# Optimization experiments

Measured on AMD Instinct MI355X. Metric: run time of the kernel, lower is better.

## Reference

```python
import jax, jax.numpy as jnp
import numpy as np

N = 100000          # nodes
E = 3200000         # edges (avg degree 32)
C = 64              # classes
NUM_CORR = 10
ALPHA_CORR = 0.979
NUM_SMOOTH = 10
ALPHA_SMOOTH = 0.756


def setup_inputs() -> dict:
    key = jax.random.key(0)
    k1, k2, k3, k4, k5 = jax.random.split(key, 5)
    # soft predictions: rows sum to 1 (asserted in the torch code)
    y_soft = jax.nn.softmax(jax.random.normal(k1, (N, C), dtype=jnp.float32), axis=-1)
    labels = jax.random.randint(k2, (N,), 0, C)
    y_true = jax.nn.one_hot(labels, C, dtype=jnp.float32)
    src = jax.random.randint(k3, (E,), 0, N)
    dst = jax.random.randint(k4, (E,), 0, N)
    mask = jax.random.uniform(k5, (N,)) < 0.5
    return {"y_soft": y_soft, "y_true": y_true, "src": src, "dst": dst, "mask": mask}


def _propagate(y, src, dst, norm, num_layers, alpha, lo, hi):
    # DAD: y <- clip(last + alpha * D^-1/2 A D^-1/2 y, lo, hi) repeated
    last = (1.0 - alpha) * y
    for _ in range(num_layers):
        y = norm * y                                            # D^-1/2 y
        h = jax.ops.segment_sum(y[src], dst, num_segments=N)    # A (SpMM via copy_u/sum)
        y = alpha * h * norm                                    # alpha D^-1/2 (.)
        y = jnp.clip(last + y, lo, hi)                          # post_step clamp
    return y


def reference(y_soft, y_true, src, dst, mask):
    dt = y_soft.dtype
    degs = jnp.clip(jax.ops.segment_sum(jnp.ones((E,), dt), dst, num_segments=N), 1.0, None)
    norm = (degs ** -0.5)[:, None]                              # [N,1]
    m = mask[:, None]

    # ---- correct (autoscale=True) ----
    error = jnp.where(m, y_true - y_soft, jnp.zeros((), dt))    # zero off-mask
    smoothed_error = _propagate(error, src, dst, norm, NUM_CORR, ALPHA_CORR, -1.0, 1.0)
    numel = jnp.sum(mask).astype(dt)
    sigma = jnp.sum(jnp.abs(error)) / numel                     # error is 0 off-mask
    scale = sigma / jnp.sum(jnp.abs(smoothed_error), axis=1, keepdims=True)
    scale = jnp.where(jnp.isinf(scale) | (scale > 1000.0), jnp.ones((), dt), scale)
    result = y_soft + scale * smoothed_error
    result = jnp.where(jnp.isnan(result), y_soft, result)

    # ---- smooth ----
    y = jnp.where(m, y_true, result)                            # y_soft[mask] = y_true
    out = _propagate(y, src, dst, norm, NUM_SMOOTH, ALPHA_SMOOTH, 0.0, 1.0)
    return out
```

## Files before the change

### kernel.cpp

```cpp
#include <hip/hip_runtime.h>
#include <hip/hip_bf16.h>

#define NN 100000
#define EE 3200000
#define CC 64
#define NC (NN*CC)
#define ERR_BLOCKS 6250
#define NB 391
#define TILE 8192
#define NTILE 391

__device__ __forceinline__ float ldf(const void* p, long i, int isbf) {
    if (isbf) {
        unsigned int u = ((const unsigned short*)p)[i];
        return __uint_as_float(u << 16);
    }
    return ((const float*)p)[i];
}

__device__ __forceinline__ float wave_sum(float a) {
    for (int m = 1; m < 64; m <<= 1) a += __shfl_xor(a, m, 64);
    return a;
}

__device__ __forceinline__ unsigned pack_bf16(float a, float b) {
    unsigned ua = __float_as_uint(a); ua = (ua + 0x7FFFu + ((ua >> 16) & 1u)) >> 16;
    unsigned ub = __float_as_uint(b); ub = (ub + 0x7FFFu + ((ub >> 16) & 1u)) >> 16;
    return ua | (ub << 16);
}

__global__ void detect_kernel(const void* ytrue, const void* mask, int* flags) {
    int t = threadIdx.x;
    const unsigned int* w = (const unsigned int*)ytrue;
    int nb = 0, nm = 0;
    for (int i = t; i < 16384; i += 256)
        if ((w[i] & 0xFFFFu) == 0x3F80u) nb = 1;
    const unsigned char* mb = (const unsigned char*)mask;
    for (int i = t; i < 4096; i += 256)
        if ((i & 3) != 0 && mb[i] != 0) nm = 1;
    if (nb) atomicOr(&flags[0], 1);
    if (nm) atomicOr(&flags[1], 1);
}

__global__ void prep_kernel(const void* ytrue, const void* mask, const int* flags,
                            int* __restrict__ label, float* __restrict__ mask01) {
    int gt = blockIdx.x * blockDim.x + threadIdx.x;
    int node = gt >> 6, lane = gt & 63;
    if (node >= NN) return;
    int isbf = flags[0];
    float tv = ldf(ytrue, (long)node * CC + lane, isbf);
    unsigned long long b = __ballot(tv > 0.5f);
    if (lane == 0) {
        label[node] = (b == 0ull) ? 0 : (__ffsll((long long)b) - 1);
        int mv = flags[1] ? (int)((const unsigned char*)mask)[node] : ((const int*)mask)[node];
        mask01[node] = mv ? 1.f : 0.f;
    }
}

__global__ void histA_kernel(const int* __restrict__ dst, int* __restrict__ bucket_tot) {
    __shared__ int hist[NB];
    int t = threadIdx.x;
    for (int b = t; b < NB; b += 256) hist[b] = 0;
    __syncthreads();
    int e0 = blockIdx.x * TILE;
    int n = EE - e0; if (n > TILE) n = TILE;
    for (int k = t; k < n; k += 256)
        atomicAdd(&hist[dst[e0 + k] >> 8], 1);
    __syncthreads();
    for (int b = t; b < NB; b += 256)
        if (hist[b]) atomicAdd(&bucket_tot[b], hist[b]);
}

__global__ void bscan_kernel(const int* __restrict__ bucket_tot,
                             int* __restrict__ bucket_base, int* __restrict__ bucket_fill) {
    int t = threadIdx.x;
    __shared__ int sm[512];
    int v = (t < NB) ? bucket_tot[t] : 0;
    sm[t] = v; __syncthreads();
    for (int off = 1; off < 512; off <<= 1) {
        int x = (t >= off) ? sm[t - off] : 0;
        __syncthreads();
        sm[t] += x;
        __syncthreads();
    }
    int ex = sm[t] - v;
    if (t <= NB) { bucket_base[t] = ex; bucket_fill[t] = ex; }
}

__global__ void __launch_bounds__(512)
binA_kernel(const int* __restrict__ src, const int* __restrict__ dst,
            int* __restrict__ bucket_fill, uint2* __restrict__ tmp) {
    __shared__ uint2 stage[TILE];
    __shared__ int hist[512], hofs[512], curL[512], gbase[512];
    __shared__ int sm[512];
    int t = threadIdx.x;
    int e0 = blockIdx.x * TILE;
    int n = EE - e0; if (n > TILE) n = TILE;

    hist[t] = 0;
    __syncthreads();
    for (int k = t; k < n; k += 512)
        atomicAdd(&hist[dst[e0 + k] >> 8], 1);
    __syncthreads();
    int v = hist[t];
    sm[t] = v; __syncthreads();
    for (int off = 1; off < 512; off <<= 1) {
        int x = (t >= off) ? sm[t - off] : 0;
        __syncthreads();
        sm[t] += x;
        __syncthreads();
    }
    hofs[t] = sm[t] - v;
    curL[t] = sm[t] - v;
    __syncthreads();
    for (int k = t; k < n; k += 512) {
        int s = src[e0 + k], d = dst[e0 + k];
        int b = d >> 8;
        int p = atomicAdd(&curL[b], 1);
        stage[p] = make_uint2((unsigned)s, (unsigned)d);
    }
    if (t < NB) {
        int c = hist[t];
        gbase[t] = c ? atomicAdd(&bucket_fill[t], c) : 0;
    }
    __syncthreads();
    for (int k = t; k < n; k += 512) {
        uint2 pr = stage[k];
        int b = (int)(pr.y >> 8);
        tmp[gbase[b] + (k - hofs[b])] = pr;
    }
}

__global__ void __launch_bounds__(256)
csrB_kernel(const uint2* __restrict__ tmp, const int* __restrict__ bucket_base,
            int* __restrict__ row_ptr, float* __restrict__ norm, int* __restrict__ csr_src) {
    __shared__ int deg[256], cur[256], sm[256];
    int t = threadIdx.x, b = blockIdx.x;
    int ebeg = bucket_base[b], eend = bucket_base[b + 1];
    deg[t] = 0;
    __syncthreads();
    for (int i = ebeg + t; i < eend; i += 256)
        atomicAdd(&deg[tmp[i].y & 255u], 1);
    __syncthreads();
    int v = deg[t];
    sm[t] = v; __syncthreads();
    for (int off = 1; off < 256; off <<= 1) {
        int x = (t >= off) ? sm[t - off] : 0;
        __syncthreads();
        sm[t] += x;
        __syncthreads();
    }
    int lofs = sm[t] - v;
    int node = b * 256 + t;
    if (node < NN) {
        row_ptr[node] = ebeg + lofs;
        int d = v; if (d < 1) d = 1;
        norm[node] = rsqrtf((float)d);
    }
    if (b == NB - 1 && t == 0) row_ptr[NN] = EE;
    cur[t] = lofs;
    __syncthreads();
    for (int i = ebeg + t; i < eend; i += 256) {
        uint2 pr = tmp[i];
        int p = atomicAdd(&cur[pr.y & 255u], 1);
        csr_src[ebeg + p] = (int)pr.x;
    }
}

__global__ void err_kernel(const void* ysoft, const int* flags, const int* __restrict__ label,
                           const float* __restrict__ mask01, const float* __restrict__ norm,
                           float* __restrict__ base, unsigned* __restrict__ curn,
                           float* __restrict__ err_part) {
    int i4 = blockIdx.x * 256 + threadIdx.x;
    int node = i4 >> 4;
    int isbf = flags[0];
    float m = mask01[node];
    int lab = label[node];
    float nrm = norm[node];
    int c0 = (i4 & 15) * 4;
    float4 e;
    if (isbf) {
        ushort4 u = ((const ushort4*)ysoft)[i4];
        e.x = __uint_as_float((unsigned)u.x << 16);
        e.y = __uint_as_float((unsigned)u.y << 16);
        e.z = __uint_as_float((unsigned)u.z << 16);
        e.w = __uint_as_float((unsigned)u.w << 16);
    } else {
        e = ((const float4*)ysoft)[i4];
    }
    e.x = (m != 0.f) ? ((c0 + 0 == lab) ? 1.f : 0.f) - e.x : 0.f;
    e.y = (m != 0.f) ? ((c0 + 1 == lab) ? 1.f : 0.f) - e.y : 0.f;
    e.z = (m != 0.f) ? ((c0 + 2 == lab) ? 1.f : 0.f) - e.z : 0.f;
    e.w = (m != 0.f) ? ((c0 + 3 == lab) ? 1.f : 0.f) - e.w : 0.f;
    ((float4*)base)[i4] = e;
    ((uint2*)curn)[i4] = make_uint2(pack_bf16(e.x * nrm, e.y * nrm),
                                    pack_bf16(e.z * nrm, e.w * nrm));
    float a = fabsf(e.x) + fabsf(e.y) + fabsf(e.z) + fabsf(e.w);
    a = wave_sum(a);
    __shared__ float sm[4];
    if ((threadIdx.x & 63) == 0) sm[threadIdx.x >> 6] = a;
    __syncthreads();
    if (threadIdx.x == 0) err_part[blockIdx.x] = sm[0] + sm[1] + sm[2] + sm[3];
}

__global__ void reduce_kernel(const float* __restrict__ mask01,
                              const float* __restrict__ err_part, float* __restrict__ scal) {
    int t = threadIdx.x;
    float s0 = 0.f, s1 = 0.f;
    for (int i = t; i < NN; i += 1024) s0 += mask01[i];
    for (int i = t; i < ERR_BLOCKS; i += 1024) s1 += err_part[i];
    __shared__ float a0[1024], a1[1024];
    a0[t] = s0; a1[t] = s1; __syncthreads();
    for (int s = 512; s > 0; s >>= 1) {
        if (t < s) { a0[t] += a0[t + s]; a1[t] += a1[t + s]; }
        __syncthreads();
    }
    if (t == 0) { scal[0] = a0[0]; scal[1] = a1[0]; }
}

__global__ void gather_kernel(const int* __restrict__ row_ptr, const int* __restrict__ csr_src,
                              const unsigned* __restrict__ curn, const float* __restrict__ base,
                              const float* __restrict__ norm, void* __restrict__ out,
                              float* __restrict__ rowsum, const int* flags,
                              float alpha, float lo, float hi, int mode) {
    int gt = blockIdx.x * blockDim.x + threadIdx.x;
    int node = gt >> 6, lane = gt & 63;
    if (node >= NN) return;
    int hl = lane & 31;
    int half = lane >> 5;
    int beg = row_ptr[node], end = row_ptr[node + 1];

    float nrm = norm[node];
    long i2 = (long)node * 32 + hl;
    float2 b2;
    {
        const float* bp = base + i2 * 2;
        b2.x = __builtin_nontemporal_load(bp);
        b2.y = __builtin_nontemporal_load(bp + 1);
    }

    float acc0 = 0.f, acc1 = 0.f, acc2 = 0.f, acc3 = 0.f;
    for (int eb = beg; eb < end; eb += 64) {
        int ne = end - eb; if (ne > 64) ne = 64;
        int sv = (eb + lane < end) ? __builtin_nontemporal_load(csr_src + eb + lane) : 0;
        int j = 0;
        for (; j + 15 < ne; j += 16) {
            int s0 = __shfl(sv, j + 0  + half, 64);
            int s1 = __shfl(sv, j + 2  + half, 64);
            int s2 = __shfl(sv, j + 4  + half, 64);
            int s3 = __shfl(sv, j + 6  + half, 64);
            int s4 = __shfl(sv, j + 8  + half, 64);
            int s5 = __shfl(sv, j + 10 + half, 64);
            int s6 = __shfl(sv, j + 12 + half, 64);
            int s7 = __shfl(sv, j + 14 + half, 64);
            unsigned w0 = curn[(long)s0 * 32 + hl];
            unsigned w1 = curn[(long)s1 * 32 + hl];
            unsigned w2 = curn[(long)s2 * 32 + hl];
            unsigned w3 = curn[(long)s3 * 32 + hl];
            unsigned w4 = curn[(long)s4 * 32 + hl];
            unsigned w5 = curn[(long)s5 * 32 + hl];
            unsigned w6 = curn[(long)s6 * 32 + hl];
            unsigned w7 = curn[(long)s7 * 32 + hl];
            acc0 += __uint_as_float(w0 << 16) + __uint_as_float(w2 << 16)
                  + __uint_as_float(w4 << 16) + __uint_as_float(w6 << 16);
            acc1 += __uint_as_float(w0 & 0xFFFF0000u) + __uint_as_float(w2 & 0xFFFF0000u)
                  + __uint_as_float(w4 & 0xFFFF0000u) + __uint_as_float(w6 & 0xFFFF0000u);
            acc2 += __uint_as_float(w1 << 16) + __uint_as_float(w3 << 16)
                  + __uint_as_float(w5 << 16) + __uint_as_float(w7 << 16);
            acc3 += __uint_as_float(w1 & 0xFFFF0000u) + __uint_as_float(w3 & 0xFFFF0000u)
                  + __uint_as_float(w5 & 0xFFFF0000u) + __uint_as_float(w7 & 0xFFFF0000u);
        }
        for (; j + 7 < ne; j += 8) {
            int s0 = __shfl(sv, j + 0 + half, 64);
            int s1 = __shfl(sv, j + 2 + half, 64);
            int s2 = __shfl(sv, j + 4 + half, 64);
            int s3 = __shfl(sv, j + 6 + half, 64);
            unsigned w0 = curn[(long)s0 * 32 + hl];
            unsigned w1 = curn[(long)s1 * 32 + hl];
            unsigned w2 = curn[(long)s2 * 32 + hl];
            unsigned w3 = curn[(long)s3 * 32 + hl];
            acc0 += __uint_as_float(w0 << 16) + __uint_as_float(w2 << 16);
            acc1 += __uint_as_float(w0 & 0xFFFF0000u) + __uint_as_float(w2 & 0xFFFF0000u);
            acc2 += __uint_as_float(w1 << 16) + __uint_as_float(w3 << 16);
            acc3 += __uint_as_float(w1 & 0xFFFF0000u) + __uint_as_float(w3 & 0xFFFF0000u);
        }
        for (; j < ne; j += 2) {
            int jj = j + half;
            float wt = (jj < ne) ? 1.f : 0.f;
            int s = __shfl(sv, (jj < ne) ? jj : j, 64);
            unsigned w = curn[(long)s * 32 + hl];
            acc0 += wt * __uint_as_float(w << 16);
            acc1 += wt * __uint_as_float(w & 0xFFFF0000u);
        }
    }
    acc0 += acc2; acc1 += acc3;
    acc0 += __shfl_xor(acc0, 32, 64);
    acc1 += __shfl_xor(acc1, 32, 64);

    float v0 = (1.f - alpha) * b2.x + alpha * nrm * acc0;
    float v1 = (1.f - alpha) * b2.y + alpha * nrm * acc1;
    v0 = v0 < lo ? lo : (v0 > hi ? hi : v0);
    v1 = v1 < lo ? lo : (v1 > hi ? hi : v1);

    if (mode == 1) {
        float contrib = (lane < 32) ? (fabsf(v0) + fabsf(v1)) : 0.f;
        float rs = wave_sum(contrib);
        if (lane == 0) rowsum[node] = rs;
        if (lane < 32) {
            float* op = (float*)out + i2 * 2;
            __builtin_nontemporal_store(v0, op);
            __builtin_nontemporal_store(v1, op + 1);
        }
    } else if (mode == 0) {
        if (lane < 32)
            __builtin_nontemporal_store(pack_bf16(v0 * nrm, v1 * nrm), (unsigned*)out + i2);
    } else {
        if (lane < 32) {
            if (flags[0]) __builtin_nontemporal_store(pack_bf16(v0, v1), (unsigned*)out + i2);
            else {
                float* op = (float*)out + i2 * 2;
                __builtin_nontemporal_store(v0, op);
                __builtin_nontemporal_store(v1, op + 1);
            }
        }
    }
}

__global__ void y0_kernel(const void* ysoft, const int* flags, const int* __restrict__ label,
                          const float* __restrict__ mask01, const float* __restrict__ rowsum,
                          const float* __restrict__ scal,
                          const float* __restrict__ norm, const float* __restrict__ smoothed,
                          float* __restrict__ base, unsigned* __restrict__ curn) {
    int i4 = blockIdx.x * 256 + threadIdx.x;
    int node = i4 >> 4;
    int isbf = flags[0];
    float m = mask01[node];
    int lab = label[node];
    float nrm = norm[node];
    float sigma = scal[1] / scal[0];
    float sc = sigma / rowsum[node];
    if (isinf(sc) || sc > 1000.f) sc = 1.f;
    int c0 = (i4 & 15) * 4;
    float4 ys;
    if (isbf) {
        ushort4 u = ((const ushort4*)ysoft)[i4];
        ys.x = __uint_as_float((unsigned)u.x << 16);
        ys.y = __uint_as_float((unsigned)u.y << 16);
        ys.z = __uint_as_float((unsigned)u.z << 16);
        ys.w = __uint_as_float((unsigned)u.w << 16);
    } else {
        ys = ((const float4*)ysoft)[i4];
    }
    float4 sm = ((const float4*)smoothed)[i4];
    float rx = ys.x + sc * sm.x; if (isnan(rx)) rx = ys.x;
    float ry = ys.y + sc * sm.y; if (isnan(ry)) ry = ys.y;
    float rz = ys.z + sc * sm.z; if (isnan(rz)) rz = ys.z;
    float rw = ys.w + sc * sm.w; if (isnan(rw)) rw = ys.w;
    float4 y;
    y.x = (m != 0.f) ? ((c0 + 0 == lab) ? 1.f : 0.f) : rx;
    y.y = (m != 0.f) ? ((c0 + 1 == lab) ? 1.f : 0.f) : ry;
    y.z = (m != 0.f) ? ((c0 + 2 == lab) ? 1.f : 0.f) : rz;
    y.w = (m != 0.f) ? ((c0 + 3 == lab) ? 1.f : 0.f) : rw;
    ((float4*)base)[i4] = y;
    ((uint2*)curn)[i4] = make_uint2(pack_bf16(y.x * nrm, y.y * nrm),
                                    pack_bf16(y.z * nrm, y.w * nrm));
}

extern "C" void kernel_launch(void* const* d_in, const int* in_sizes, int n_in,
                              void* d_out, int out_size, void* d_ws, size_t ws_size,
                              hipStream_t stream) {
    const void* ysoft = d_in[0];
    const void* ytrue = d_in[1];
    const int* src = (const int*)d_in[2];
    const int* dst = (const int*)d_in[3];
    const void* mask = d_in[4];

    char* ws = (char*)d_ws;
    int*   flags       = (int*)ws;
    float* scal        = (float*)(ws + 64);
    int*   bucket_tot  = (int*)(ws + 4096);
    size_t ZERO_BYTES  = 16384;
    int*   bucket_base = (int*)(ws + 16384);
    int*   bucket_fill = (int*)(ws + 20480);
    float* err_part    = (float*)(ws + 24576);

    size_t off = 24576 + (size_t)ERR_BLOCKS * 4;
    off = (off + 255) & ~(size_t)255;
    int*   label   = (int*)(ws + off);   off += (size_t)NN * 4;
    float* mask01  = (float*)(ws + off); off += (size_t)NN * 4;
    float* norm    = (float*)(ws + off); off += (size_t)NN * 4;
    float* rowsum  = (float*)(ws + off); off += (size_t)NN * 4;
    int*   row_ptr = (int*)(ws + off);   off += (size_t)(NN + 1) * 4;
    off = (off + 255) & ~(size_t)255;
    int*   csr_src = (int*)(ws + off);   off += (size_t)EE * 4;
    off = (off + 255) & ~(size_t)255;
    float*    base     = (float*)(ws + off);    off += (size_t)NC * 4;
    float*    smoothed = (float*)(ws + off);    off += (size_t)NC * 4;
    unsigned* bufA     = (unsigned*)(ws + off); off += (size_t)NC * 2;
    unsigned* bufB     = (unsigned*)(ws + off); off += (size_t)NC * 2;
    uint2* tmp = (uint2*)base;

    hipMemsetAsync(ws, 0, ZERO_BYTES, stream);

    detect_kernel<<<1, 256, 0, stream>>>(ytrue, mask, flags);
    prep_kernel<<<(NN * 64 + 255) / 256, 256, 0, stream>>>(ytrue, mask, flags, label, mask01);
    histA_kernel<<<NTILE, 256, 0, stream>>>(dst, bucket_tot);
    bscan_kernel<<<1, 512, 0, stream>>>(bucket_tot, bucket_base, bucket_fill);
    binA_kernel<<<NTILE, 512, 0, stream>>>(src, dst, bucket_fill, tmp);
    csrB_kernel<<<NB, 256, 0, stream>>>(tmp, bucket_base, row_ptr, norm, csr_src);
    err_kernel<<<ERR_BLOCKS, 256, 0, stream>>>(ysoft, flags, label, mask01, norm, base, bufA, err_part);
    reduce_kernel<<<1, 1024, 0, stream>>>(mask01, err_part, scal);

    const int gather_blocks = (NN * 64 + 255) / 256;

    unsigned* cur = bufA; unsigned* nxt = bufB;
    for (int l = 0; l < 10; l++) {
        int mode = (l < 9) ? 0 : 1;
        void* o = (l < 9) ? (void*)nxt : (void*)smoothed;
        gather_kernel<<<gather_blocks, 256, 0, stream>>>(row_ptr, csr_src, cur, base, norm, o,
                                                         rowsum, flags, 0.979f, -1.f, 1.f, mode);
        unsigned* t = cur; cur = nxt; nxt = t;
    }

    y0_kernel<<<ERR_BLOCKS, 256, 0, stream>>>(ysoft, flags, label, mask01, rowsum, scal, norm,
                                              smoothed, base, bufA);

    cur = bufA; nxt = bufB;
    for (int l = 0; l < 10; l++) {
        int mode = (l < 9) ? 0 : 3;
        void* o = (l < 9) ? (void*)nxt : (void*)d_out;
        gather_kernel<<<gather_blocks, 256, 0, stream>>>(row_ptr, csr_src, cur, base, norm, o,
                                                         rowsum, flags, 0.756f, 0.f, 1.f, mode);
        unsigned* t = cur; cur = nxt; nxt = t;
    }
}
```

Before: 1.453 ms.

## Sort edges by source then destination and store base term in bf16

The CSR build becomes a two-pass bucket sort: edges are first binned by source, then re-binned by destination using per-tile offsets. Chunked loops with barriers make the ordering close to stable, so each row's neighbour list ends up roughly sorted by source. That sorting aims to improve cache locality of the gather's feature reads. Separately, the (1-alpha)*base term is now stored as bf16 instead of fp32, halving that read in every gather iteration. The cost is extra preprocessing kernels and a tileHist buffer, plus some accuracy loss in the residual term.

Result: no change. 1.467 ms (+0.9%).

```diff
diff --git a/kernel.cpp b/kernel.cpp
--- a/kernel.cpp
+++ b/kernel.cpp
@@ -57,7 +57,7 @@
     }
 }
 
-__global__ void histA_kernel(const int* __restrict__ dst, int* __restrict__ bucket_tot) {
+__global__ void histS_kernel(const int* __restrict__ src, int* __restrict__ sbucket_tot) {
     __shared__ int hist[NB];
     int t = threadIdx.x;
     for (int b = t; b < NB; b += 256) hist[b] = 0;
@@ -65,17 +65,17 @@
     int e0 = blockIdx.x * TILE;
     int n = EE - e0; if (n > TILE) n = TILE;
     for (int k = t; k < n; k += 256)
-        atomicAdd(&hist[dst[e0 + k] >> 8], 1);
+        atomicAdd(&hist[src[e0 + k] >> 8], 1);
     __syncthreads();
     for (int b = t; b < NB; b += 256)
-        if (hist[b]) atomicAdd(&bucket_tot[b], hist[b]);
-}
-
-__global__ void bscan_kernel(const int* __restrict__ bucket_tot,
-                             int* __restrict__ bucket_base, int* __restrict__ bucket_fill) {
+        if (hist[b]) atomicAdd(&sbucket_tot[b], hist[b]);
+}
+
+__global__ void bscan_kernel(const int* __restrict__ tot,
+                             int* __restrict__ basep, int* __restrict__ fillp) {
     int t = threadIdx.x;
     __shared__ int sm[512];
-    int v = (t < NB) ? bucket_tot[t] : 0;
+    int v = (t < NB) ? tot[t] : 0;
     sm[t] = v; __syncthreads();
     for (int off = 1; off < 512; off <<= 1) {
         int x = (t >= off) ? sm[t - off] : 0;
@@ -84,12 +84,12 @@
         __syncthreads();
     }
     int ex = sm[t] - v;
-    if (t <= NB) { bucket_base[t] = ex; bucket_fill[t] = ex; }
+    if (t <= NB) { basep[t] = ex; fillp[t] = ex; }
 }
 
 __global__ void __launch_bounds__(512)
-binA_kernel(const int* __restrict__ src, const int* __restrict__ dst,
-            int* __restrict__ bucket_fill, uint2* __restrict__ tmp) {
+binS_kernel(const int* __restrict__ src, const int* __restrict__ dst,
+            int* __restrict__ sbucket_fill, uint2* __restrict__ tmp2) {
     __shared__ uint2 stage[TILE];
     __shared__ int hist[512], hofs[512], curL[512], gbase[512];
     __shared__ int sm[512];
@@ -100,7 +100,7 @@
     hist[t] = 0;
     __syncthreads();
     for (int k = t; k < n; k += 512)
-        atomicAdd(&hist[dst[e0 + k] >> 8], 1);
+        atomicAdd(&hist[src[e0 + k] >> 8], 1);
     __syncthreads();
     int v = hist[t];
     sm[t] = v; __syncthreads();
@@ -115,15 +115,89 @@
     __syncthreads();
     for (int k = t; k < n; k += 512) {
         int s = src[e0 + k], d = dst[e0 + k];
-        int b = d >> 8;
+        int b = s >> 8;
         int p = atomicAdd(&curL[b], 1);
         stage[p] = make_uint2((unsigned)s, (unsigned)d);
     }
     if (t < NB) {
         int c = hist[t];
-        gbase[t] = c ? atomicAdd(&bucket_fill[t], c) : 0;
-    }
-    __syncthreads();
+        gbase[t] = c ? atomicAdd(&sbucket_fill[t], c) : 0;
+    }
+    __syncthreads();
+    for (int k = t; k < n; k += 512) {
+        uint2 pr = stage[k];
+        int b = (int)(pr.x >> 8);
+        tmp2[gbase[b] + (k - hofs[b])] = pr;
+    }
+}
+
+__global__ void histT_kernel(const uint2* __restrict__ tmp2, int* __restrict__ tileHist) {
+    __shared__ int hist[NB];
+    int t = threadIdx.x, tile = blockIdx.x;
+    for (int b = t; b < NB; b += 256) hist[b] = 0;
+    __syncthreads();
+    int e0 = tile * TILE;
+    int n = EE - e0; if (n > TILE) n = TILE;
+    for (int k = t; k < n; k += 256)
+        atomicAdd(&hist[tmp2[e0 + k].y >> 8], 1);
+    __syncthreads();
+    for (int b = t; b < NB; b += 256)
+        tileHist[b * NTILE + tile] = hist[b];
+}
+
+__global__ void scanT_kernel(int* __restrict__ tileHist, int* __restrict__ colsum) {
+    int t = threadIdx.x, b = blockIdx.x;
+    int* col = tileHist + b * NTILE;
+    __shared__ int sm[512];
+    int v = (t < NTILE) ? col[t] : 0;
+    sm[t] = v; __syncthreads();
+    for (int off = 1; off < 512; off <<= 1) {
+        int x = (t >= off) ? sm[t - off] : 0;
+        __syncthreads();
+        sm[t] += x;
+        __syncthreads();
+    }
+    if (t < NTILE) col[t] = sm[t] - v;
+    if (t == 511) colsum[b] = sm[511];
+}
+
+__global__ void __launch_bounds__(512)
+binT_kernel(const uint2* __restrict__ tmp2, const int* __restrict__ bucket_base,
+            const int* __restrict__ tileOfs, uint2* __restrict__ tmp) {
+    __shared__ uint2 stage[TILE];
+    __shared__ int hist[512], hofs[512], curL[512], gbase[512];
+    __shared__ int sm[512];
+    int t = threadIdx.x, tile = blockIdx.x;
+    int e0 = tile * TILE;
+    int n = EE - e0; if (n > TILE) n = TILE;
+
+    hist[t] = 0;
+    __syncthreads();
+    for (int k = t; k < n; k += 512)
+        atomicAdd(&hist[tmp2[e0 + k].y >> 8], 1);
+    __syncthreads();
+    int v = hist[t];
+    sm[t] = v; __syncthreads();
+    for (int off = 1; off < 512; off <<= 1) {
+        int x = (t >= off) ? sm[t - off] : 0;
+        __syncthreads();
+        sm[t] += x;
+        __syncthreads();
+    }
+    hofs[t] = sm[t] - v;
+    curL[t] = sm[t] - v;
+    if (t < NB) gbase[t] = bucket_base[t] + tileOfs[t * NTILE + tile];
+    __syncthreads();
+    for (int k0 = 0; k0 < n; k0 += 512) {
+        int k = k0 + t;
+        if (k < n) {
+            uint2 pr = tmp2[e0 + k];
+            int b = (int)(pr.y >> 8);
+            int p = atomicAdd(&curL[b], 1);
+            stage[p] = pr;
+        }
+        __syncthreads();
+    }
     for (int k = t; k < n; k += 512) {
         uint2 pr = stage[k];
         int b = (int)(pr.y >> 8);
@@ -160,16 +234,20 @@
     if (b == NB - 1 && t == 0) row_ptr[NN] = EE;
     cur[t] = lofs;
     __syncthreads();
-    for (int i = ebeg + t; i < eend; i += 256) {
-        uint2 pr = tmp[i];
-        int p = atomicAdd(&cur[pr.y & 255u], 1);
-        csr_src[ebeg + p] = (int)pr.x;
+    for (int i0 = ebeg; i0 < eend; i0 += 256) {
+        int i = i0 + t;
+        if (i < eend) {
+            uint2 pr = tmp[i];
+            int p = atomicAdd(&cur[pr.y & 255u], 1);
+            csr_src[ebeg + p] = (int)pr.x;
+        }
+        __syncthreads();
     }
 }
 
 __global__ void err_kernel(const void* ysoft, const int* flags, const int* __restrict__ label,
                            const float* __restrict__ mask01, const float* __restrict__ norm,
-                           float* __restrict__ base, unsigned* __restrict__ curn,
+                           unsigned* __restrict__ base_u, unsigned* __restrict__ curn,
                            float* __restrict__ err_part) {
     int i4 = blockIdx.x * 256 + threadIdx.x;
     int node = i4 >> 4;
@@ -192,7 +270,7 @@
     e.y = (m != 0.f) ? ((c0 + 1 == lab) ? 1.f : 0.f) - e.y : 0.f;
     e.z = (m != 0.f) ? ((c0 + 2 == lab) ? 1.f : 0.f) - e.z : 0.f;
     e.w = (m != 0.f) ? ((c0 + 3 == lab) ? 1.f : 0.f) - e.w : 0.f;
-    ((float4*)base)[i4] = e;
+    ((uint2*)base_u)[i4] = make_uint2(pack_bf16(e.x, e.y), pack_bf16(e.z, e.w));
     ((uint2*)curn)[i4] = make_uint2(pack_bf16(e.x * nrm, e.y * nrm),
                                     pack_bf16(e.z * nrm, e.w * nrm));
     float a = fabsf(e.x) + fabsf(e.y) + fabsf(e.z) + fabsf(e.w);
@@ -219,7 +297,7 @@
 }
 
 __global__ void gather_kernel(const int* __restrict__ row_ptr, const int* __restrict__ csr_src,
-                              const unsigned* __restrict__ curn, const float* __restrict__ base,
+                              const unsigned* __restrict__ curn, const unsigned* __restrict__ base_u,
                               const float* __restrict__ norm, void* __restrict__ out,
                               float* __restrict__ rowsum, const int* flags,
                               float alpha, float lo, float hi, int mode) {
@@ -232,12 +310,9 @@
 
     float nrm = norm[node];
     long i2 = (long)node * 32 + hl;
-    float2 b2;
-    {
-        const float* bp = base + i2 * 2;
-        b2.x = __builtin_nontemporal_load(bp);
-        b2.y = __builtin_nontemporal_load(bp + 1);
-    }
+    unsigned bu = __builtin_nontemporal_load(base_u + i2);
+    float b0 = __uint_as_float(bu << 16);
+    float b1 = __uint_as_float(bu & 0xFFFF0000u);
 
     float acc0 = 0.f, acc1 = 0.f, acc2 = 0.f, acc3 = 0.f;
     for (int eb = beg; eb < end; eb += 64) {
@@ -297,8 +372,8 @@
     acc0 += __shfl_xor(acc0, 32, 64);
     acc1 += __shfl_xor(acc1, 32, 64);
 
-    float v0 = (1.f - alpha) * b2.x + alpha * nrm * acc0;
-    float v1 = (1.f - alpha) * b2.y + alpha * nrm * acc1;
+    float v0 = (1.f - alpha) * b0 + alpha * nrm * acc0;
+    float v1 = (1.f - alpha) * b1 + alpha * nrm * acc1;
     v0 = v0 < lo ? lo : (v0 > hi ? hi : v0);
     v1 = v1 < lo ? lo : (v1 > hi ? hi : v1);
 
@@ -330,7 +405,7 @@
                           const float* __restrict__ mask01, const float* __restrict__ rowsum,
                           const float* __restrict__ scal,
                           const float* __restrict__ norm, const float* __restrict__ smoothed,
-                          float* __restrict__ base, unsigned* __restrict__ curn) {
+                          unsigned* __restrict__ base_u, unsigned* __restrict__ curn) {
     int i4 = blockIdx.x * 256 + threadIdx.x;
     int node = i4 >> 4;
     int isbf = flags[0];
@@ -361,7 +436,7 @@
     y.y = (m != 0.f) ? ((c0 + 1 == lab) ? 1.f : 0.f) : ry;
     y.z = (m != 0.f) ? ((c0 + 2 == lab) ? 1.f : 0.f) : rz;
     y.w = (m != 0.f) ? ((c0 + 3 == lab) ? 1.f : 0.f) : rw;
-    ((float4*)base)[i4] = y;
+    ((uint2*)base_u)[i4] = make_uint2(pack_bf16(y.x, y.y), pack_bf16(y.z, y.w));
     ((uint2*)curn)[i4] = make_uint2(pack_bf16(y.x * nrm, y.y * nrm),
                                     pack_bf16(y.z * nrm, y.w * nrm));
 }
@@ -376,15 +451,20 @@
     const void* mask = d_in[4];
 
     char* ws = (char*)d_ws;
-    int*   flags       = (int*)ws;
-    float* scal        = (float*)(ws + 64);
-    int*   bucket_tot  = (int*)(ws + 4096);
-    size_t ZERO_BYTES  = 16384;
-    int*   bucket_base = (int*)(ws + 16384);
-    int*   bucket_fill = (int*)(ws + 20480);
-    float* err_part    = (float*)(ws + 24576);
-
-    size_t off = 24576 + (size_t)ERR_BLOCKS * 4;
+    int*   flags        = (int*)ws;
+    float* scal         = (float*)(ws + 64);
+    int*   sbucket_tot  = (int*)(ws + 4096);
+    size_t ZERO_BYTES   = 8192;
+    int*   sbucket_base = (int*)(ws + 8192);
+    int*   sbucket_fill = (int*)(ws + 12288);
+    int*   bucket_base  = (int*)(ws + 16384);
+    int*   bucket_fill  = (int*)(ws + 20480);
+    int*   colsum       = (int*)(ws + 24576);
+    float* err_part     = (float*)(ws + 28672);
+
+    size_t off = 28672 + (size_t)ERR_BLOCKS * 4;
+    off = (off + 255) & ~(size_t)255;
+    int*   tileHist = (int*)(ws + off);  off += (size_t)NB * NTILE * 4;
     off = (off + 255) & ~(size_t)255;
     int*   label   = (int*)(ws + off);   off += (size_t)NN * 4;
     float* mask01  = (float*)(ws + off); off += (size_t)NN * 4;
@@ -394,21 +474,26 @@
     off = (off + 255) & ~(size_t)255;
     int*   csr_src = (int*)(ws + off);   off += (size_t)EE * 4;
     off = (off + 255) & ~(size_t)255;
-    float*    base     = (float*)(ws + off);    off += (size_t)NC * 4;
-    float*    smoothed = (float*)(ws + off);    off += (size_t)NC * 4;
+    unsigned* base_u   = (unsigned*)(ws + off); off += (size_t)NC * 2;
     unsigned* bufA     = (unsigned*)(ws + off); off += (size_t)NC * 2;
     unsigned* bufB     = (unsigned*)(ws + off); off += (size_t)NC * 2;
-    uint2* tmp = (uint2*)base;
+    float*    smoothed = (float*)(ws + off);    off += (size_t)NC * 4;
+    uint2* tmp  = (uint2*)base_u;
+    uint2* tmp2 = (uint2*)smoothed;
 
     hipMemsetAsync(ws, 0, ZERO_BYTES, stream);
 
     detect_kernel<<<1, 256, 0, stream>>>(ytrue, mask, flags);
     prep_kernel<<<(NN * 64 + 255) / 256, 256, 0, stream>>>(ytrue, mask, flags, label, mask01);
-    histA_kernel<<<NTILE, 256, 0, stream>>>(dst, bucket_tot);
-    bscan_kernel<<<1, 512, 0, stream>>>(bucket_tot, bucket_base, bucket_fill);
-    binA_kernel<<<NTILE, 512, 0, stream>>>(src, dst, bucket_fill, tmp);
+    histS_kernel<<<NTILE, 256, 0, stream>>>(src, sbucket_tot);
+    bscan_kernel<<<1, 512, 0, stream>>>(sbucket_tot, sbucket_base, sbucket_fill);
+    binS_kernel<<<NTILE, 512, 0, stream>>>(src, dst, sbucket_fill, tmp2);
+    histT_kernel<<<NTILE, 256, 0, stream>>>(tmp2, tileHist);
+    scanT_kernel<<<NB, 512, 0, stream>>>(tileHist, colsum);
+    bscan_kernel<<<1, 512, 0, stream>>>(colsum, bucket_base, bucket_fill);
+    binT_kernel<<<NTILE, 512, 0, stream>>>(tmp2, bucket_base, tileHist, tmp);
     csrB_kernel<<<NB, 256, 0, stream>>>(tmp, bucket_base, row_ptr, norm, csr_src);
-    err_kernel<<<ERR_BLOCKS, 256, 0, stream>>>(ysoft, flags, label, mask01, norm, base, bufA, err_part);
+    err_kernel<<<ERR_BLOCKS, 256, 0, stream>>>(ysoft, flags, label, mask01, norm, base_u, bufA, err_part);
     reduce_kernel<<<1, 1024, 0, stream>>>(mask01, err_part, scal);
 
     const int gather_blocks = (NN * 64 + 255) / 256;
@@ -417,19 +502,19 @@
     for (int l = 0; l < 10; l++) {
         int mode = (l < 9) ? 0 : 1;
         void* o = (l < 9) ? (void*)nxt : (void*)smoothed;
-        gather_kernel<<<gather_blocks, 256, 0, stream>>>(row_ptr, csr_src, cur, base, norm, o,
+        gather_kernel<<<gather_blocks, 256, 0, stream>>>(row_ptr, csr_src, cur, base_u, norm, o,
                                                          rowsum, flags, 0.979f, -1.f, 1.f, mode);
         unsigned* t = cur; cur = nxt; nxt = t;
     }
 
     y0_kernel<<<ERR_BLOCKS, 256, 0, stream>>>(ysoft, flags, label, mask01, rowsum, scal, norm,
-                                              smoothed, base, bufA);
+                                              smoothed, base_u, bufA);
 
     cur = bufA; nxt = bufB;
     for (int l = 0; l < 10; l++) {
         int mode = (l < 9) ? 0 : 3;
         void* o = (l < 9) ? (void*)nxt : (void*)d_out;
-        gather_kernel<<<gather_blocks, 256, 0, stream>>>(row_ptr, csr_src, cur, base, norm, o,
+        gather_kernel<<<gather_blocks, 256, 0, stream>>>(row_ptr, csr_src, cur, base_u, norm, o,
                                                          rowsum, flags, 0.756f, 0.f, 1.f, mode);
         unsigned* t = cur; cur = nxt; nxt = t;
     }
```
